# Optimization experiments

Measured on AMD Instinct MI355X. Metric: run time of the kernel, lower is better.

## Reference

```python
import jax, jax.numpy as jnp
import numpy as np


def _make_grid(h, w, stride=1):
    """Vectorized port of gen_grid_coordinates_exp. Returns (1, 3*Ho, 3*Wo, 2) float32,
    last dim = (x_norm, y_norm) in [-1,1] (torch grid_sample convention)."""
    rows = np.arange(0, h, stride)
    cols = np.arange(0, w, stride)
    theta = -((rows + 0.5) / h * np.pi - np.pi / 2)          # (Ho,)
    phi = (cols + 0.5) / w * 2 * np.pi - np.pi               # (Wo,)
    dtheta = np.pi / h
    dphi = 2 * np.pi / w
    # 3x3 tangent-plane offsets (du: horizontal, dv: vertical), per get_exp_duv
    du = np.tan(dphi) * np.array([[-1., 0., 1.]] * 3)                      # (3,3)
    dv = np.tan(dtheta) * np.array([[1., 1., 1.], [0., 0., 0.], [-1., -1., -1.]])
    T = theta[:, None, None, None]   # (Ho,1,1,1)
    P = phi[None, :, None, None]     # (1,Wo,1,1)
    u_x = -du * np.sin(P) - dv * np.sin(T) * np.cos(P)       # (Ho,Wo,3,3)
    u_y = du * np.cos(P) - dv * np.sin(T) * np.sin(P)
    u_z = dv * np.cos(T) + np.zeros_like(u_x)
    u_norm = np.sqrt(u_x ** 2 + u_y ** 2 + u_z ** 2)
    u_div = np.where(u_norm == 0, 1.0, u_norm)
    c, s = np.cos(u_norm), np.sin(u_norm)
    ex = np.cos(T) * np.cos(P) * c + u_x / u_div * s
    ey = np.cos(T) * np.sin(P) * c + u_y / u_div * s
    ez = np.sin(T) * c + u_z / u_div * s
    new_phi = np.arctan2(ey, ex)
    new_theta = np.arcsin(np.clip(ez, -1.0, 1.0))
    new_r = (-new_theta + np.pi / 2) * h / np.pi - 0.5
    new_c = ((new_phi + np.pi) * w / (2 * np.pi) - 0.5 + w) % w
    # kernel center samples the original integer pixel exactly
    new_r[:, :, 1, 1] = rows[:, None]
    new_c[:, :, 1, 1] = cols[None, :]
    gx = new_c * 2.0 / w - 1.0
    gy = new_r * 2.0 / h - 1.0
    grid = np.stack([gx, gy], axis=-1)                        # (Ho,Wo,3,3,2)
    Ho, Wo = len(rows), len(cols)
    grid = grid.transpose(0, 2, 1, 3, 4).reshape(1, Ho * 3, Wo * 3, 2)
    return grid.astype(np.float32)


def _grid_sample_bilinear(x, grid):
    """torch.nn.functional.grid_sample(mode='bilinear', padding='zeros', align_corners=False).
    x: (B,C,H,W); grid: (1,Hg,Wg,2) shared across batch."""
    B, C, H, W = x.shape
    gx = grid[0, ..., 0]
    gy = grid[0, ..., 1]
    Hg, Wg = gx.shape
    ix = ((gx + 1.0) * W - 1.0) * 0.5   # unnormalize, align_corners=False
    iy = ((gy + 1.0) * H - 1.0) * 0.5
    x0 = jnp.floor(ix); x1 = x0 + 1.0
    y0 = jnp.floor(iy); y1 = y0 + 1.0
    xf = x.reshape(B, C, H * W)

    def corner(xc, yc, wgt):
        valid = (xc >= 0) & (xc < W) & (yc >= 0) & (yc < H)
        xi = jnp.clip(xc, 0, W - 1).astype(jnp.int32)
        yi = jnp.clip(yc, 0, H - 1).astype(jnp.int32)
        idx = (yi * W + xi).reshape(-1)                      # (Hg*Wg,)
        w_eff = (wgt * valid.astype(wgt.dtype)).reshape(-1)  # zero-pad OOB
        return xf[:, :, idx] * w_eff                          # (B,C,Hg*Wg)

    out = (corner(x0, y0, (x1 - ix) * (y1 - iy))
           + corner(x1, y0, (ix - x0) * (y1 - iy))
           + corner(x0, y1, (x1 - ix) * (iy - y0))
           + corner(x1, y1, (ix - x0) * (iy - y0)))
    return out.reshape(B, C, Hg, Wg)


def setup_inputs() -> dict:
    key = jax.random.key(0)
    k1, k2 = jax.random.split(key)
    B, Cin, Cout, H, W = 4, 128, 256, 128, 256
    x = jax.random.normal(k1, (B, Cin, H, W), dtype=jnp.float32)
    # kaiming_uniform_(a=sqrt(5)) -> U(-1/sqrt(fan_in), 1/sqrt(fan_in)), fan_in = Cin*9
    bound = 1.0 / np.sqrt(Cin * 9)
    weight = jax.random.uniform(k2, (Cout, Cin, 3, 3), dtype=jnp.float32,
                                minval=-bound, maxval=bound)
    bias = jnp.zeros((Cout,), dtype=jnp.float32)
    grid = jnp.asarray(_make_grid(H, W, stride=1))  # (1, 3H, 3W, 2)
    return {"x": x, "weight": weight, "bias": bias, "grid": grid}


def reference(x, weight, bias, grid):
    sampled = _grid_sample_bilinear(x, grid)                 # (B,C,3H,3W)
    out = jax.lax.conv_general_dilated(
        sampled, weight, window_strides=(3, 3), padding='VALID',
        dimension_numbers=('NCHW', 'OIHW', 'NCHW'))          # (B,Cout,H,W)
    return out + bias[None, :, None, None]
```

## Files before the change

### kernel.cpp

```cpp
#include <hip/hip_runtime.h>


#define Hh   128
#define Ww   256
#define HWp  (Hh*Ww)
#define CIN  128
#define COUT 256
#define KTOT 1152
#define NPTS (384*768)
#define BM   128
#define BN   256
#define BK   32
#define NKS  (KTOT/BK)

typedef __attribute__((ext_vector_type(8))) __bf16 bf16x8;
typedef __attribute__((ext_vector_type(4))) float  f32x4;

__global__ void build_table(const float* __restrict__ grid,
                            int2* __restrict__ tI, float4* __restrict__ tW) {
    int g = blockIdx.x * 256 + threadIdx.x;
    if (g >= NPTS) return;
    int hh = g / 768, ww = g - hh * 768;
    int ho = hh / 3, ii = hh - 3 * ho;
    int wo = ww / 3, jj = ww - 3 * wo;

    float gx = grid[2 * g + 0];
    float gy = grid[2 * g + 1];
    float ix = ((gx + 1.0f) * (float)Ww - 1.0f) * 0.5f;
    float iy = ((gy + 1.0f) * (float)Hh - 1.0f) * 0.5f;
    float x0f = floorf(ix), y0f = floorf(iy);
    int x0 = (int)x0f, y0 = (int)y0f;
    float wx1 = ix - x0f, wx0 = 1.0f - wx1;
    float wy1 = iy - y0f, wy0 = 1.0f - wy1;

    float wyt = (y0 >= 0 && y0 < Hh) ? wy0 : 0.0f;
    float wyb = (y0 + 1 >= 0 && y0 + 1 < Hh) ? wy1 : 0.0f;
    int r0 = min(max(y0, 0), Hh - 1);
    int r1 = min(max(y0 + 1, 0), Hh - 1);

    int xb; float cw0, cw1;
    if (x0 < 0)            { xb = 0;      cw0 = wx1; cw1 = 0.0f; }
    else if (x0 > Ww - 2)  { xb = Ww - 2; cw0 = 0.0f; cw1 = wx0; }
    else                   { xb = x0;     cw0 = wx0; cw1 = wx1; }

    int e = (ho * Ww + wo) * 9 + ii * 3 + jj;
    tI[e] = make_int2(r0 * Ww + xb, r1 * Ww + xb);
    tW[e] = make_float4(cw0 * wyt, cw1 * wyt, cw0 * wyb, cw1 * wyb);
}

__global__ void conv_w(const float* __restrict__ w, __bf16* __restrict__ wt) {
    int o = blockIdx.x * 256 + threadIdx.x;
    if (o >= NKS * COUT * BK) return;
    int kk = o & (BK - 1);
    int n  = (o >> 5) & (COUT - 1);
    int ks = o >> 13;
    int kp = ks * BK + kk;
    int ij = kp >> 7;
    int ci = kp & (CIN - 1);
    wt[o] = (__bf16)w[n * KTOT + ci * 9 + ij];
}

__global__ __launch_bounds__(512, 4) void sphconv_gemm(
    const float* __restrict__ x, const __bf16* __restrict__ wt,
    const float* __restrict__ bias, const int2* __restrict__ tI,
    const float4* __restrict__ tW, float* __restrict__ out) {

    __shared__ int2   sTI[BM * 9];
    __shared__ float4 sTW[BM * 9];
    __shared__ __align__(16) __bf16 sA[BM * 40];
    __shared__ __align__(16) __bf16 sB[BN * 40];

    const int t   = threadIdx.x;
    const int m0  = blockIdx.x * BM;
    const int b   = m0 >> 15;
    const int sp0 = m0 & (HWp - 1);
    const float* xb_ = x + (size_t)b * (CIN * HWp);

    for (int e = t; e < BM * 9; e += 512) {
        sTI[e] = tI[sp0 * 9 + e];
        sTW[e] = tW[sp0 * 9 + e];
    }

    const int lane = t & 63;
    const int wid  = t >> 6;
    const int wrow = wid >> 2;
    const int wcol = wid & 3;
    const int quad = lane >> 4;
    const int l16  = lane & 15;

    const int mr_s = t & 127;
    const int kg   = t >> 7;

    f32x4 acc[4][4];
#pragma unroll
    for (int r = 0; r < 4; ++r)
#pragma unroll
        for (int c = 0; c < 4; ++c) {
            f32x4 z = {0.0f, 0.0f, 0.0f, 0.0f};
            acc[r][c] = z;
        }

    __syncthreads();

    for (int ks = 0; ks < NKS; ++ks) {
        const int ij  = ks >> 2;
        const int ci0 = (ks & 3) * 32 + kg * 8;
        const int2   o  = sTI[mr_s * 9 + ij];
        const float4 wv = sTW[mr_s * 9 + ij];
        const float* img = xb_ + (size_t)ci0 * HWp;
        bf16x8 av;
#pragma unroll
        for (int j = 0; j < 8; ++j) {
            float2 p0 = *(const float2*)(img + o.x);
            float2 p1 = *(const float2*)(img + o.y);
            av[j] = (__bf16)(p0.x * wv.x + p0.y * wv.y + p1.x * wv.z + p1.y * wv.w);
            img += HWp;
        }
        *(bf16x8*)(&sA[mr_s * 40 + kg * 8]) = av;

        {
            const __bf16* src = wt + ks * (COUT * BK) + t * 16;
            bf16x8 v0 = *(const bf16x8*)(src);
            bf16x8 v1 = *(const bf16x8*)(src + 8);
            int n  = t >> 1;
            int kq = (t & 1) * 16;
            *(bf16x8*)(&sB[n * 40 + kq])     = v0;
            *(bf16x8*)(&sB[n * 40 + kq + 8]) = v1;
        }
        __syncthreads();

        bf16x8 af[4], bfr[4];
#pragma unroll
        for (int r = 0; r < 4; ++r)
            af[r] = *(const bf16x8*)(&sA[(wrow * 64 + r * 16 + l16) * 40 + quad * 8]);
#pragma unroll
        for (int c = 0; c < 4; ++c)
            bfr[c] = *(const bf16x8*)(&sB[(wcol * 64 + c * 16 + l16) * 40 + quad * 8]);
#pragma unroll
        for (int r = 0; r < 4; ++r)
#pragma unroll
            for (int c = 0; c < 4; ++c)
                acc[r][c] = __builtin_amdgcn_mfma_f32_16x16x32_bf16(
                    af[r], bfr[c], acc[r][c], 0, 0, 0);
        __syncthreads();
    }

#pragma unroll
    for (int c = 0; c < 4; ++c) {
        int n = wcol * 64 + c * 16 + l16;
        float bv = bias[n];
        float* outn = out + (((size_t)(b * COUT + n)) << 15) + sp0;
#pragma unroll
        for (int r = 0; r < 4; ++r) {
            int mbase = wrow * 64 + r * 16 + quad * 4;
            float4 v = make_float4(acc[r][c][0] + bv, acc[r][c][1] + bv,
                                   acc[r][c][2] + bv, acc[r][c][3] + bv);
            *(float4*)(&outn[mbase]) = v;
        }
    }
}

extern "C" void kernel_launch(void* const* d_in, const int* in_sizes, int n_in,
                              void* d_out, int out_size, void* d_ws, size_t ws_size,
                              hipStream_t stream) {
    const float* x    = (const float*)d_in[0];
    const float* w    = (const float*)d_in[1];
    const float* bias = (const float*)d_in[2];
    const float* grid = (const float*)d_in[3];
    float* out = (float*)d_out;

    char* ws = (char*)d_ws;
    int2*   tI = (int2*)(ws);
    float4* tW = (float4*)(ws + 2359296);
    __bf16* wt = (__bf16*)(ws + 7077888);

    build_table<<<(NPTS + 255) / 256, 256, 0, stream>>>(grid, tI, tW);
    conv_w<<<(NKS * COUT * BK + 255) / 256, 256, 0, stream>>>(w, wt);
    sphconv_gemm<<<(4 * HWp) / BM, 512, 0, stream>>>(x, wt, bias, tI, tW, out);
}
```

Before: 393.5 us.

## Prefetch next K-step gathers into registers and reorder K loop tap-major

Issues the global gather loads for the next K-step (bilinear corner pixels and bf16 weight slices) into registers before the barrier, so they overlap the MFMA work of the current step. The K dimension is reordered so the 9 kernel taps iterate innermost over each 32-channel block, with the weight repack kernel changed to match. The __syncthreads calls become raw s_barrier plus an lgkmcnt wait, so the barrier no longer waits on outstanding global loads. The cost is higher register pressure from holding 16 float2 values plus the weight vectors at launch_bounds(512,4), which could cause spills or lower occupancy.

Result: slower. 520.6 us (+32.3%).

```diff
diff --git a/kernel.cpp b/kernel.cpp
--- a/kernel.cpp
+++ b/kernel.cpp
@@ -54,9 +54,8 @@
     int kk = o & (BK - 1);
     int n  = (o >> 5) & (COUT - 1);
     int ks = o >> 13;
-    int kp = ks * BK + kk;
-    int ij = kp >> 7;
-    int ci = kp & (CIN - 1);
+    int ij = ks % 9;
+    int ci = (ks / 9) * 32 + kk;
     wt[o] = (__bf16)w[n * KTOT + ci * 9 + ij];
 }
 
@@ -90,6 +89,8 @@
 
     const int mr_s = t & 127;
     const int kg   = t >> 7;
+    const int wn   = t >> 1;
+    const int wkq  = (t & 1) * 16;
 
     f32x4 acc[4][4];
 #pragma unroll
@@ -102,32 +103,56 @@
 
     __syncthreads();
 
+    float2 px[8], py[8];
+    bf16x8 pb0, pb1;
+    float4 wv;
+    {
+        const int2 o = sTI[mr_s * 9 + 0];
+        wv = sTW[mr_s * 9 + 0];
+        const float* img = xb_ + (size_t)(kg * 8) * HWp;
+#pragma unroll
+        for (int j = 0; j < 8; ++j) {
+            px[j] = *(const float2*)(img + o.x);
+            py[j] = *(const float2*)(img + o.y);
+            img += HWp;
+        }
+        const __bf16* src = wt + t * 16;
+        pb0 = *(const bf16x8*)(src);
+        pb1 = *(const bf16x8*)(src + 8);
+    }
+
+    int ij = 0, cb = 0;
     for (int ks = 0; ks < NKS; ++ks) {
-        const int ij  = ks >> 2;
-        const int ci0 = (ks & 3) * 32 + kg * 8;
-        const int2   o  = sTI[mr_s * 9 + ij];
-        const float4 wv = sTW[mr_s * 9 + ij];
-        const float* img = xb_ + (size_t)ci0 * HWp;
         bf16x8 av;
 #pragma unroll
-        for (int j = 0; j < 8; ++j) {
-            float2 p0 = *(const float2*)(img + o.x);
-            float2 p1 = *(const float2*)(img + o.y);
-            av[j] = (__bf16)(p0.x * wv.x + p0.y * wv.y + p1.x * wv.z + p1.y * wv.w);
-            img += HWp;
-        }
+        for (int j = 0; j < 8; ++j)
+            av[j] = (__bf16)(px[j].x * wv.x + px[j].y * wv.y +
+                             py[j].x * wv.z + py[j].y * wv.w);
         *(bf16x8*)(&sA[mr_s * 40 + kg * 8]) = av;
 
-        {
-            const __bf16* src = wt + ks * (COUT * BK) + t * 16;
-            bf16x8 v0 = *(const bf16x8*)(src);
-            bf16x8 v1 = *(const bf16x8*)(src + 8);
-            int n  = t >> 1;
-            int kq = (t & 1) * 16;
-            *(bf16x8*)(&sB[n * 40 + kq])     = v0;
-            *(bf16x8*)(&sB[n * 40 + kq + 8]) = v1;
-        }
-        __syncthreads();
+        *(bf16x8*)(&sB[wn * 40 + wkq])     = pb0;
+        *(bf16x8*)(&sB[wn * 40 + wkq + 8]) = pb1;
+
+        int ij2 = ij + 1, cb2 = cb;
+        if (ij2 == 9) { ij2 = 0; cb2 += 32; }
+        if (ks + 1 < NKS) {
+            const int2 o = sTI[mr_s * 9 + ij2];
+            wv = sTW[mr_s * 9 + ij2];
+            const float* img = xb_ + (size_t)(cb2 + kg * 8) * HWp;
+#pragma unroll
+            for (int j = 0; j < 8; ++j) {
+                px[j] = *(const float2*)(img + o.x);
+                py[j] = *(const float2*)(img + o.y);
+                img += HWp;
+            }
+            const __bf16* src = wt + (ks + 1) * (COUT * BK) + t * 16;
+            pb0 = *(const bf16x8*)(src);
+            pb1 = *(const bf16x8*)(src + 8);
+        }
+        ij = ij2; cb = cb2;
+
+        asm volatile("s_waitcnt lgkmcnt(0)" ::: "memory");
+        __builtin_amdgcn_s_barrier();
 
         bf16x8 af[4], bfr[4];
 #pragma unroll
@@ -142,7 +167,9 @@
             for (int c = 0; c < 4; ++c)
                 acc[r][c] = __builtin_amdgcn_mfma_f32_16x16x32_bf16(
                     af[r], bfr[c], acc[r][c], 0, 0, 0);
-        __syncthreads();
+
+        asm volatile("s_waitcnt lgkmcnt(0)" ::: "memory");
+        __builtin_amdgcn_s_barrier();
     }
 
 #pragma unroll
```
